# Performance work log

Measured on AMD Instinct MI355X. Metric: run time of the kernel, lower is better.

The kernel has to match this reference:

```python
import jax, jax.numpy as jnp
import numpy as np

B, S, D_MODEL, D_K, D_V, H = 4, 2048, 1024, 1024, 1024, 16


def setup_inputs() -> dict:
    key = jax.random.key(0)
    ks = jax.random.split(key, 8)
    std_qk = np.sqrt(2.0 / (D_MODEL + D_K)).astype(np.float32)
    std_v = np.sqrt(2.0 / (D_MODEL + D_V)).astype(np.float32)
    std_o = np.sqrt(2.0 / (D_V + D_MODEL)).astype(np.float32)  # xavier normal
    return {
        "Q": jax.random.normal(ks[0], (B, S, D_MODEL), jnp.float32),
        "K": jax.random.normal(ks[1], (B, S, D_MODEL), jnp.float32),
        "V": jax.random.normal(ks[2], (B, S, D_MODEL), jnp.float32),
        "Wq": jax.random.normal(ks[3], (D_MODEL, D_K), jnp.float32) * std_qk,
        "bq": jnp.zeros((D_K,), jnp.float32),
        "Wk": jax.random.normal(ks[4], (D_MODEL, D_K), jnp.float32) * std_qk,
        "bk": jnp.zeros((D_K,), jnp.float32),
        "Wv": jax.random.normal(ks[5], (D_MODEL, D_V), jnp.float32) * std_v,
        "bv": jnp.zeros((D_V,), jnp.float32),
        "Wo": jax.random.normal(ks[6], (D_V, D_MODEL), jnp.float32) * std_o,
        "bo": jnp.zeros((D_MODEL,), jnp.float32),
    }


def reference(Q, K, V, Wq, bq, Wk, bk, Wv, bv, Wo, bo):
    b, s, _ = Q.shape
    hd = D_K // H  # per-head dim
    # separate QKV projections
    q = (Q @ Wq + bq).reshape(b, s, H, hd)
    k = (K @ Wk + bk).reshape(b, s, H, hd)
    v = (V @ Wv + bv).reshape(b, s, H, D_V // H)
    # scaled dot-product attention per head
    scale = 1.0 / jnp.sqrt(jnp.asarray(hd, Q.dtype))
    scores = jnp.einsum("bqhd,bkhd->bhqk", q, k) * scale
    attn = jax.nn.softmax(scores, axis=-1)
    o = jnp.einsum("bhqk,bkhd->bqhd", attn, v).reshape(b, s, D_V)
    # output projection
    return o @ Wo + bo
```

## Files before the change

### kernel.cpp

```cpp
#include <hip/hip_runtime.h>
#include <hip/hip_bf16.h>
#include <stdint.h>


#define B_  4
#define S_  2048
#define DM  1024
#define H_  16
#define HD  64
#define BH  (B_ * H_)

typedef __attribute__((ext_vector_type(8))) short short8;
typedef __attribute__((ext_vector_type(4))) float f32x4;

union U8 { short8 v; ushort u[8]; };

__device__ __forceinline__ ushort f2bf(float f) {
  union { float f; uint32_t i; } x; x.f = f;
  uint32_t r = (x.i + 0x7FFFu + ((x.i >> 16) & 1u)) >> 16;
  return (ushort)r;
}

__device__ __forceinline__ uint32_t cvt_pk_bf16(float a, float b) {
  uint32_t r;
  asm("v_cvt_pk_bf16_f32 %0, %1, %2" : "=v"(r) : "v"(a), "v"(b));
  return r;
}

__device__ __forceinline__ float exp2f_fast(float x) {
  float r;
  asm("v_exp_f32 %0, %1" : "=v"(r) : "v"(x));
  return r;
}

__device__ __forceinline__ void glds16(const ushort* g, ushort* l) {
  __builtin_amdgcn_global_load_lds(
      (const __attribute__((address_space(1))) void*)g,
      (__attribute__((address_space(3))) void*)l, 16, 0, 0);
}

#define MAX3(a, b, c) fmaxf(fmaxf((a), (b)), (c))

__global__ __launch_bounds__(256) void transposeW4(
    const float* __restrict__ s0, const float* __restrict__ s1,
    const float* __restrict__ s2, const float* __restrict__ s3,
    ushort* __restrict__ dbase) {
  __shared__ __align__(16) ushort tile[64][72];
  const int t = threadIdx.x;
  const int bx = blockIdx.x & 15;
  const int by = blockIdx.x >> 4;
  const int wsel = blockIdx.y;
  const float* src = wsel == 0 ? s0 : (wsel == 1 ? s1 : (wsel == 2 ? s2 : s3));
  ushort* dst = dbase + (size_t)wsel * 1024 * 1024;
#pragma unroll
  for (int i = 0; i < 2; i++) {
    int e = (i * 256 + t) * 8;
    int r = e >> 6, c = e & 63;
    const float* sp = src + (size_t)(by * 64 + r) * 1024 + bx * 64 + c;
    float4 a = ((const float4*)sp)[0];
    float4 b = ((const float4*)sp)[1];
    tile[r][c + 0] = f2bf(a.x); tile[r][c + 1] = f2bf(a.y);
    tile[r][c + 2] = f2bf(a.z); tile[r][c + 3] = f2bf(a.w);
    tile[r][c + 4] = f2bf(b.x); tile[r][c + 5] = f2bf(b.y);
    tile[r][c + 6] = f2bf(b.z); tile[r][c + 7] = f2bf(b.w);
  }
  __syncthreads();
#pragma unroll
  for (int i = 0; i < 2; i++) {
    int e = (i * 256 + t) * 8;
    int r = e >> 6, c = e & 63;
    U8 st;
#pragma unroll
    for (int j = 0; j < 8; j++) st.u[j] = tile[c + j][r];
    *(short8*)(dst + (size_t)(bx * 64 + r) * 1024 + by * 64 + c) = st.v;
  }
}

__global__ __launch_bounds__(256, 2) void gemm_qkv(
    const float* __restrict__ Qa, const float* __restrict__ Ka, const float* __restrict__ Va,
    const ushort* __restrict__ WT,
    const float* __restrict__ bq, const float* __restrict__ bk, const float* __restrict__ bv,
    ushort* __restrict__ qws, ushort* __restrict__ kws, ushort* __restrict__ vt) {
  __shared__ __align__(16) ushort lA[128 * 32];
  __shared__ __align__(16) ushort lB[128 * 32];
  const int z = blockIdx.z;
  const float* Ap = z == 0 ? Qa : (z == 1 ? Ka : Va);
  const ushort* BT = WT + (size_t)z * 1024 * 1024;
  const float* bias = z == 0 ? bq : (z == 1 ? bk : bv);
  const float oscale = z == 0 ? 0.18033688f : 1.0f;
  const int t = threadIdx.x;
  const int lane = t & 63;
  const int w = t >> 6;
  const int wr = w >> 1, wc = w & 1;
  const int bm0 = blockIdx.x * 128;
  const int bn0 = blockIdx.y * 128;
  f32x4 acc[4][4] = {};

  const int arow = t >> 2;
  const int acol = (t & 3) * 8;
  const float* fA0 = Ap + (size_t)(bm0 + arow) * 1024 + acol;
  const float* fA1 = Ap + (size_t)(bm0 + 64 + arow) * 1024 + acol;
  const ushort* gB0 = BT + (size_t)(bn0 + arow) * 1024 + acol;
  const ushort* gB1 = BT + (size_t)(bn0 + 64 + arow) * 1024 + acol;

  for (int k0 = 0; k0 < 1024; k0 += 32) {
    if (k0) __syncthreads();
    float4 x0 = ((const float4*)(fA0 + k0))[0];
    float4 x1 = ((const float4*)(fA0 + k0))[1];
    float4 y0 = ((const float4*)(fA1 + k0))[0];
    float4 y1 = ((const float4*)(fA1 + k0))[1];
    union { short8 v; uint32_t u[4]; } s0, s1;
    s0.u[0] = cvt_pk_bf16(x0.x, x0.y); s0.u[1] = cvt_pk_bf16(x0.z, x0.w);
    s0.u[2] = cvt_pk_bf16(x1.x, x1.y); s0.u[3] = cvt_pk_bf16(x1.z, x1.w);
    s1.u[0] = cvt_pk_bf16(y0.x, y0.y); s1.u[1] = cvt_pk_bf16(y0.z, y0.w);
    s1.u[2] = cvt_pk_bf16(y1.x, y1.y); s1.u[3] = cvt_pk_bf16(y1.z, y1.w);
    *(short8*)&lA[t * 8] = s0.v;
    *(short8*)&lA[2048 + t * 8] = s1.v;
    glds16(gB0 + k0, &lB[t * 8]);
    glds16(gB1 + k0, &lB[2048 + t * 8]);
    __syncthreads();
    short8 af[4], bf[4];
#pragma unroll
    for (int i = 0; i < 4; i++)
      af[i] = *(const short8*)&lA[(wr * 64 + i * 16 + (lane & 15)) * 32 + (lane >> 4) * 8];
#pragma unroll
    for (int j = 0; j < 4; j++)
      bf[j] = *(const short8*)&lB[(wc * 64 + j * 16 + (lane & 15)) * 32 + (lane >> 4) * 8];
#pragma unroll
    for (int i = 0; i < 4; i++)
#pragma unroll
      for (int j = 0; j < 4; j++)
        acc[i][j] = __builtin_amdgcn_mfma_f32_16x16x32_bf16(af[i], bf[j], acc[i][j], 0, 0, 0);
  }

  const int r0 = (lane >> 4) * 4;
#pragma unroll
  for (int j = 0; j < 4; j++) {
    const int col = bn0 + wc * 64 + j * 16 + (lane & 15);
    const float bc = bias[col];
#pragma unroll
    for (int i = 0; i < 4; i++) {
      const int row = bm0 + wr * 64 + i * 16 + r0;
      const int bb = row >> 11, s = row & 2047;
      const int hh = col >> 6, d = col & 63;
      if (z == 2) {
        uint32_t p01 = cvt_pk_bf16(acc[i][j][0] + bc, acc[i][j][1] + bc);
        uint32_t p23 = cvt_pk_bf16(acc[i][j][2] + bc, acc[i][j][3] + bc);
        ushort* vtb = vt + (((size_t)bb * H_ + hh) * HD + d) * (size_t)S_;
        const int sc = (s & 63) >> 2;
        *(uint2*)(vtb + (s & ~63) + ((sc ^ (d & 15)) << 2)) = (uint2){p01, p23};
      } else {
        ushort* dst = z == 0 ? qws : kws;
#pragma unroll
        for (int r = 0; r < 4; r++) {
          float val = (acc[i][j][r] + bc) * oscale;
          dst[(((size_t)bb * H_ + hh) * S_ + (s + r)) * HD + d] = f2bf(val);
        }
      }
    }
  }
}

__global__ __launch_bounds__(256, 2) void gemm_out(
    const ushort* __restrict__ Ap, const ushort* __restrict__ BT,
    const float* __restrict__ bias, float* __restrict__ Cp) {
  __shared__ __align__(16) ushort lA[128 * 32];
  __shared__ __align__(16) ushort lB[128 * 32];
  const int t = threadIdx.x;
  const int lane = t & 63;
  const int w = t >> 6;
  const int wr = w >> 1, wc = w & 1;
  const int bm0 = blockIdx.x * 128;
  const int bn0 = blockIdx.y * 128;
  f32x4 acc[4][4] = {};

  const int arow = t >> 2;
  const int acol = (t & 3) * 8;
  const ushort* gA0 = Ap + (size_t)(bm0 + arow) * 1024 + acol;
  const ushort* gA1 = Ap + (size_t)(bm0 + 64 + arow) * 1024 + acol;
  const ushort* gB0 = BT + (size_t)(bn0 + arow) * 1024 + acol;
  const ushort* gB1 = BT + (size_t)(bn0 + 64 + arow) * 1024 + acol;

  for (int k0 = 0; k0 < 1024; k0 += 32) {
    if (k0) __syncthreads();
    glds16(gA0 + k0, &lA[t * 8]);
    glds16(gA1 + k0, &lA[2048 + t * 8]);
    glds16(gB0 + k0, &lB[t * 8]);
    glds16(gB1 + k0, &lB[2048 + t * 8]);
    __syncthreads();
    short8 af[4], bf[4];
#pragma unroll
    for (int i = 0; i < 4; i++)
      af[i] = *(const short8*)&lA[(wr * 64 + i * 16 + (lane & 15)) * 32 + (lane >> 4) * 8];
#pragma unroll
    for (int j = 0; j < 4; j++)
      bf[j] = *(const short8*)&lB[(wc * 64 + j * 16 + (lane & 15)) * 32 + (lane >> 4) * 8];
#pragma unroll
    for (int i = 0; i < 4; i++)
#pragma unroll
      for (int j = 0; j < 4; j++)
        acc[i][j] = __builtin_amdgcn_mfma_f32_16x16x32_bf16(af[i], bf[j], acc[i][j], 0, 0, 0);
  }

  const int r0 = (lane >> 4) * 4;
#pragma unroll
  for (int j = 0; j < 4; j++) {
    const int col = bn0 + wc * 64 + j * 16 + (lane & 15);
    const float bc = bias[col];
#pragma unroll
    for (int i = 0; i < 4; i++) {
      const int row = bm0 + wr * 64 + i * 16 + r0;
#pragma unroll
      for (int r = 0; r < 4; r++)
        Cp[(size_t)(row + r) * 1024 + col] = acc[i][j][r] + bc;
    }
  }
}

__global__ __launch_bounds__(256, 2) void attn(
    const ushort* __restrict__ q, const ushort* __restrict__ k,
    const ushort* __restrict__ vt, ushort* __restrict__ o) {
  __shared__ __align__(16) ushort kbuf[2][4096];
  __shared__ __align__(16) ushort vbuf[2][4096];
  const int t = threadIdx.x;
  const int lane = t & 63;
  const int w = t >> 6;
  const int L = ((blockIdx.x & 7) << 6) + (blockIdx.x >> 3);
  const int bh = L >> 3;
  const int q0 = (L & 7) * 256;
  const int b = bh >> 4, h = bh & 15;
  const int l15 = lane & 15;
  const int g = lane >> 4;

  const ushort* kbase  = k  + (size_t)bh * S_ * HD;
  const ushort* vtbase = vt + (size_t)bh * HD * S_;

  short8 qf[4][2];
#pragma unroll
  for (int qi = 0; qi < 4; qi++) {
    const ushort* qp = q + ((size_t)bh * S_ + q0 + w * 64 + qi * 16 + l15) * HD + g * 8;
    qf[qi][0] = *(const short8*)qp;
    qf[qi][1] = *(const short8*)(qp + 32);
  }

  short8 onesf;
#pragma unroll
  for (int j = 0; j < 8; j++) onesf[j] = (short)0x3F80;

  float m_r[4] = {-1e30f, -1e30f, -1e30f, -1e30f};
  f32x4 l_acc[4];
  f32x4 o_acc[4][4];
#pragma unroll
  for (int qi = 0; qi < 4; qi++) {
    l_acc[qi] = (f32x4){0.f, 0.f, 0.f, 0.f};
#pragma unroll
    for (int cb = 0; cb < 4; cb++) o_acc[qi][cb] = (f32x4){0.f, 0.f, 0.f, 0.f};
  }

  int vo[2][2];
#pragma unroll
  for (int ks = 0; ks < 2; ks++) {
    vo[ks][0] = ((8 * ks + g) ^ l15) << 2;
    vo[ks][1] = ((8 * ks + 4 + g) ^ l15) << 2;
  }

  auto STAGE = [&](int sel_, int kv0) {
#pragma unroll
    for (int i = 0; i < 2; i++) {
      int c = i * 256 + t;
      int row = c >> 3;
      int cc = (c & 7) ^ (row & 7);
      glds16(kbase + (size_t)(kv0 + row) * HD + cc * 8, &kbuf[sel_][c * 8]);
      glds16(vtbase + (size_t)row * S_ + kv0 + (c & 7) * 8, &vbuf[sel_][c * 8]);
    }
  };

  STAGE(0, 0);
  __syncthreads();

  int sel = 0;
  for (int kv0 = 0; kv0 < S_; kv0 += 64, sel ^= 1) {
    if (kv0 + 64 < S_) STAGE(sel ^ 1, kv0 + 64);

    f32x4 sc[4][4];
#pragma unroll
    for (int qi = 0; qi < 4; qi++)
#pragma unroll
      for (int cb = 0; cb < 4; cb++) sc[qi][cb] = (f32x4){0.f, 0.f, 0.f, 0.f};
    __builtin_amdgcn_s_setprio(1);
#pragma unroll
    for (int cb = 0; cb < 4; cb++) {
      const int row = cb * 16 + l15;
      const int r7 = row & 7;
      short8 kf0 = *(const short8*)&kbuf[sel][(row * 8 + (g ^ r7)) * 8];
      short8 kf1 = *(const short8*)&kbuf[sel][(row * 8 + ((4 + g) ^ r7)) * 8];
#pragma unroll
      for (int qi = 0; qi < 4; qi++) {
        sc[qi][cb] = __builtin_amdgcn_mfma_f32_16x16x32_bf16(kf0, qf[qi][0], sc[qi][cb], 0, 0, 0);
        sc[qi][cb] = __builtin_amdgcn_mfma_f32_16x16x32_bf16(kf1, qf[qi][1], sc[qi][cb], 0, 0, 0);
      }
    }
    __builtin_amdgcn_s_setprio(0);

    union PB { short8 v; uint32_t u[4]; } pbq[4][2];
#pragma unroll
    for (int qi = 0; qi < 4; qi++) {
      const float m = m_r[qi];
#pragma unroll
      for (int cb = 0; cb < 4; cb++) {
        float p0 = exp2f_fast(sc[qi][cb][0] - m);
        float p1 = exp2f_fast(sc[qi][cb][1] - m);
        float p2 = exp2f_fast(sc[qi][cb][2] - m);
        float p3 = exp2f_fast(sc[qi][cb][3] - m);
        pbq[qi][cb >> 1].u[(cb & 1) * 2 + 0] = cvt_pk_bf16(p0, p1);
        pbq[qi][cb >> 1].u[(cb & 1) * 2 + 1] = cvt_pk_bf16(p2, p3);
      }
      float z0 = MAX3(sc[qi][0][0], sc[qi][0][1], sc[qi][0][2]);
      float z1 = MAX3(sc[qi][0][3], sc[qi][1][0], sc[qi][1][1]);
      float z2 = MAX3(sc[qi][1][2], sc[qi][1][3], sc[qi][2][0]);
      float z3 = MAX3(sc[qi][2][1], sc[qi][2][2], sc[qi][2][3]);
      float z4 = MAX3(sc[qi][3][0], sc[qi][3][1], sc[qi][3][2]);
      float mx = MAX3(MAX3(z0, z1, z2), fmaxf(z3, z4), sc[qi][3][3]);
      mx = fmaxf(mx, __shfl_xor(mx, 16));
      mx = fmaxf(mx, __shfl_xor(mx, 32));

      const float THR = 11.5415603f;
      if (!__all(mx <= m + THR)) {
        float mn = fmaxf(m, mx);
        float fct = exp2f_fast(m - mn);
        m_r[qi] = mn;
        l_acc[qi] *= fct;
#pragma unroll
        for (int cb = 0; cb < 4; cb++)
#pragma unroll
          for (int r = 0; r < 4; r++) o_acc[qi][cb][r] *= fct;
#pragma unroll
        for (int cb = 0; cb < 4; cb++) {
          float p0 = exp2f_fast(sc[qi][cb][0] - mn);
          float p1 = exp2f_fast(sc[qi][cb][1] - mn);
          float p2 = exp2f_fast(sc[qi][cb][2] - mn);
          float p3 = exp2f_fast(sc[qi][cb][3] - mn);
          pbq[qi][cb >> 1].u[(cb & 1) * 2 + 0] = cvt_pk_bf16(p0, p1);
          pbq[qi][cb >> 1].u[(cb & 1) * 2 + 1] = cvt_pk_bf16(p2, p3);
        }
      }
    }

    __builtin_amdgcn_s_setprio(1);
#pragma unroll
    for (int ks = 0; ks < 2; ks++) {
#pragma unroll
      for (int qi = 0; qi < 4; qi++)
        l_acc[qi] = __builtin_amdgcn_mfma_f32_16x16x32_bf16(onesf, pbq[qi][ks].v, l_acc[qi], 0, 0, 0);
#pragma unroll
      for (int cb = 0; cb < 4; cb++) {
        const ushort* vb = &vbuf[sel][(cb * 16 + l15) * 64];
        union { short8 v; uint2 d2[2]; } vv;
        vv.d2[0] = *(const uint2*)(vb + vo[ks][0]);
        vv.d2[1] = *(const uint2*)(vb + vo[ks][1]);
#pragma unroll
        for (int qi = 0; qi < 4; qi++)
          o_acc[qi][cb] = __builtin_amdgcn_mfma_f32_16x16x32_bf16(vv.v, pbq[qi][ks].v, o_acc[qi][cb], 0, 0, 0);
      }
    }
    __builtin_amdgcn_s_setprio(0);
    __syncthreads();
  }

#pragma unroll
  for (int qi = 0; qi < 4; qi++) {
    const float inv = 1.f / l_acc[qi][0];
    ushort* ob = o + ((size_t)b * S_ + q0 + w * 64 + qi * 16 + l15) * DM + h * HD + 4 * g;
#pragma unroll
    for (int cb = 0; cb < 4; cb++) {
      uint2 st;
      st.x = cvt_pk_bf16(o_acc[qi][cb][0] * inv, o_acc[qi][cb][1] * inv);
      st.y = cvt_pk_bf16(o_acc[qi][cb][2] * inv, o_acc[qi][cb][3] * inv);
      *(uint2*)(ob + cb * 16) = st;
    }
  }
}

extern "C" void kernel_launch(void* const* d_in, const int* in_sizes, int n_in,
                              void* d_out, int out_size, void* d_ws, size_t ws_size,
                              hipStream_t stream) {
  const float* Q  = (const float*)d_in[0];
  const float* K  = (const float*)d_in[1];
  const float* V  = (const float*)d_in[2];
  const float* Wq = (const float*)d_in[3];
  const float* bq = (const float*)d_in[4];
  const float* Wk = (const float*)d_in[5];
  const float* bk = (const float*)d_in[6];
  const float* Wv = (const float*)d_in[7];
  const float* bv = (const float*)d_in[8];
  const float* Wo = (const float*)d_in[9];
  const float* bo = (const float*)d_in[10];
  float* out = (float*)d_out;
  ushort* ws = (ushort*)d_ws;

  const size_t WN = (size_t)1024 * 1024;
  const size_t PN = (size_t)B_ * S_ * DM;
  ushort* wT  = ws;
  ushort* woT = ws + 3 * WN;
  ushort* qws = ws + 4 * WN;
  ushort* kws = qws + PN;
  ushort* ows = kws + PN;
  ushort* vt  = (ushort*)d_out;

  transposeW4<<<dim3(256, 4), 256, 0, stream>>>(Wq, Wk, Wv, Wo, wT);

  gemm_qkv<<<dim3(64, 8, 3), 256, 0, stream>>>(Q, K, V, wT, bq, bk, bv, qws, kws, vt);

  attn<<<BH * 8, 256, 0, stream>>>(qws, kws, vt, ows);

  gemm_out<<<dim3(64, 8), 256, 0, stream>>>(ows, woT, bo, out);
}
```

Baseline: 196.4 us.

## Prefetch next A tile in projection GEMM and double KV tile size in attention

In the projection GEMM, the fp32 A-tile loads for the next k-step are issued into registers right after the barrier, so global latency overlaps the MFMA work. In attention, each staged K/V tile grows from 64 to 128 keys and is processed as two 64-key halves, halving the number of barriers and stage calls per sequence. This doubles the attention kernel's LDS footprint to 64KB per block, which may reduce occupancy, and the prefetch adds register pressure to the GEMM. The V tile layout changes to 128-wide rows, and the existing XOR read pattern is reused within each half.

Result: faster. 190.9 us (-2.8%).

```diff
diff --git a/kernel.cpp b/kernel.cpp
--- a/kernel.cpp
+++ b/kernel.cpp
@@ -103,22 +103,29 @@
   const ushort* gB0 = BT + (size_t)(bn0 + arow) * 1024 + acol;
   const ushort* gB1 = BT + (size_t)(bn0 + 64 + arow) * 1024 + acol;
 
+  float4 px0 = ((const float4*)fA0)[0];
+  float4 px1 = ((const float4*)fA0)[1];
+  float4 py0 = ((const float4*)fA1)[0];
+  float4 py1 = ((const float4*)fA1)[1];
+
   for (int k0 = 0; k0 < 1024; k0 += 32) {
     if (k0) __syncthreads();
-    float4 x0 = ((const float4*)(fA0 + k0))[0];
-    float4 x1 = ((const float4*)(fA0 + k0))[1];
-    float4 y0 = ((const float4*)(fA1 + k0))[0];
-    float4 y1 = ((const float4*)(fA1 + k0))[1];
     union { short8 v; uint32_t u[4]; } s0, s1;
-    s0.u[0] = cvt_pk_bf16(x0.x, x0.y); s0.u[1] = cvt_pk_bf16(x0.z, x0.w);
-    s0.u[2] = cvt_pk_bf16(x1.x, x1.y); s0.u[3] = cvt_pk_bf16(x1.z, x1.w);
-    s1.u[0] = cvt_pk_bf16(y0.x, y0.y); s1.u[1] = cvt_pk_bf16(y0.z, y0.w);
-    s1.u[2] = cvt_pk_bf16(y1.x, y1.y); s1.u[3] = cvt_pk_bf16(y1.z, y1.w);
+    s0.u[0] = cvt_pk_bf16(px0.x, px0.y); s0.u[1] = cvt_pk_bf16(px0.z, px0.w);
+    s0.u[2] = cvt_pk_bf16(px1.x, px1.y); s0.u[3] = cvt_pk_bf16(px1.z, px1.w);
+    s1.u[0] = cvt_pk_bf16(py0.x, py0.y); s1.u[1] = cvt_pk_bf16(py0.z, py0.w);
+    s1.u[2] = cvt_pk_bf16(py1.x, py1.y); s1.u[3] = cvt_pk_bf16(py1.z, py1.w);
     *(short8*)&lA[t * 8] = s0.v;
     *(short8*)&lA[2048 + t * 8] = s1.v;
     glds16(gB0 + k0, &lB[t * 8]);
     glds16(gB1 + k0, &lB[2048 + t * 8]);
     __syncthreads();
+    if (k0 + 32 < 1024) {
+      px0 = ((const float4*)(fA0 + k0 + 32))[0];
+      px1 = ((const float4*)(fA0 + k0 + 32))[1];
+      py0 = ((const float4*)(fA1 + k0 + 32))[0];
+      py1 = ((const float4*)(fA1 + k0 + 32))[1];
+    }
     short8 af[4], bf[4];
 #pragma unroll
     for (int i = 0; i < 4; i++)
@@ -220,8 +227,8 @@
 __global__ __launch_bounds__(256, 2) void attn(
     const ushort* __restrict__ q, const ushort* __restrict__ k,
     const ushort* __restrict__ vt, ushort* __restrict__ o) {
-  __shared__ __align__(16) ushort kbuf[2][4096];
-  __shared__ __align__(16) ushort vbuf[2][4096];
+  __shared__ __align__(16) ushort kbuf[2][8192];
+  __shared__ __align__(16) ushort vbuf[2][8192];
   const int t = threadIdx.x;
   const int lane = t & 63;
   const int w = t >> 6;
@@ -266,12 +273,14 @@
 
   auto STAGE = [&](int sel_, int kv0) {
 #pragma unroll
-    for (int i = 0; i < 2; i++) {
+    for (int i = 0; i < 4; i++) {
       int c = i * 256 + t;
-      int row = c >> 3;
-      int cc = (c & 7) ^ (row & 7);
-      glds16(kbase + (size_t)(kv0 + row) * HD + cc * 8, &kbuf[sel_][c * 8]);
-      glds16(vtbase + (size_t)row * S_ + kv0 + (c & 7) * 8, &vbuf[sel_][c * 8]);
+      int krow = c >> 3;
+      int kcc = (c & 7) ^ (krow & 7);
+      glds16(kbase + (size_t)(kv0 + krow) * HD + kcc * 8, &kbuf[sel_][c * 8]);
+      int d = c >> 4;
+      int voff = ((c >> 3) & 1) * 64 + (c & 7) * 8;
+      glds16(vtbase + (size_t)d * S_ + kv0 + voff, &vbuf[sel_][c * 8]);
     }
   };
 
@@ -279,91 +288,94 @@
   __syncthreads();
 
   int sel = 0;
-  for (int kv0 = 0; kv0 < S_; kv0 += 64, sel ^= 1) {
-    if (kv0 + 64 < S_) STAGE(sel ^ 1, kv0 + 64);
-
-    f32x4 sc[4][4];
-#pragma unroll
-    for (int qi = 0; qi < 4; qi++)
-#pragma unroll
-      for (int cb = 0; cb < 4; cb++) sc[qi][cb] = (f32x4){0.f, 0.f, 0.f, 0.f};
-    __builtin_amdgcn_s_setprio(1);
-#pragma unroll
-    for (int cb = 0; cb < 4; cb++) {
-      const int row = cb * 16 + l15;
-      const int r7 = row & 7;
-      short8 kf0 = *(const short8*)&kbuf[sel][(row * 8 + (g ^ r7)) * 8];
-      short8 kf1 = *(const short8*)&kbuf[sel][(row * 8 + ((4 + g) ^ r7)) * 8];
+  for (int kv0 = 0; kv0 < S_; kv0 += 128, sel ^= 1) {
+    if (kv0 + 128 < S_) STAGE(sel ^ 1, kv0 + 128);
+
+#pragma unroll
+    for (int hb = 0; hb < 2; hb++) {
+      f32x4 sc[4][4];
+#pragma unroll
+      for (int qi = 0; qi < 4; qi++)
+#pragma unroll
+        for (int cb = 0; cb < 4; cb++) sc[qi][cb] = (f32x4){0.f, 0.f, 0.f, 0.f};
+      __builtin_amdgcn_s_setprio(1);
+#pragma unroll
+      for (int cb = 0; cb < 4; cb++) {
+        const int row = hb * 64 + cb * 16 + l15;
+        const int r7 = row & 7;
+        short8 kf0 = *(const short8*)&kbuf[sel][(row * 8 + (g ^ r7)) * 8];
+        short8 kf1 = *(const short8*)&kbuf[sel][(row * 8 + ((4 + g) ^ r7)) * 8];
+#pragma unroll
+        for (int qi = 0; qi < 4; qi++) {
+          sc[qi][cb] = __builtin_amdgcn_mfma_f32_16x16x32_bf16(kf0, qf[qi][0], sc[qi][cb], 0, 0, 0);
+          sc[qi][cb] = __builtin_amdgcn_mfma_f32_16x16x32_bf16(kf1, qf[qi][1], sc[qi][cb], 0, 0, 0);
+        }
+      }
+      __builtin_amdgcn_s_setprio(0);
+
+      union PB { short8 v; uint32_t u[4]; } pbq[4][2];
 #pragma unroll
       for (int qi = 0; qi < 4; qi++) {
-        sc[qi][cb] = __builtin_amdgcn_mfma_f32_16x16x32_bf16(kf0, qf[qi][0], sc[qi][cb], 0, 0, 0);
-        sc[qi][cb] = __builtin_amdgcn_mfma_f32_16x16x32_bf16(kf1, qf[qi][1], sc[qi][cb], 0, 0, 0);
-      }
-    }
-    __builtin_amdgcn_s_setprio(0);
-
-    union PB { short8 v; uint32_t u[4]; } pbq[4][2];
-#pragma unroll
-    for (int qi = 0; qi < 4; qi++) {
-      const float m = m_r[qi];
-#pragma unroll
-      for (int cb = 0; cb < 4; cb++) {
-        float p0 = exp2f_fast(sc[qi][cb][0] - m);
-        float p1 = exp2f_fast(sc[qi][cb][1] - m);
-        float p2 = exp2f_fast(sc[qi][cb][2] - m);
-        float p3 = exp2f_fast(sc[qi][cb][3] - m);
-        pbq[qi][cb >> 1].u[(cb & 1) * 2 + 0] = cvt_pk_bf16(p0, p1);
-        pbq[qi][cb >> 1].u[(cb & 1) * 2 + 1] = cvt_pk_bf16(p2, p3);
-      }
-      float z0 = MAX3(sc[qi][0][0], sc[qi][0][1], sc[qi][0][2]);
-      float z1 = MAX3(sc[qi][0][3], sc[qi][1][0], sc[qi][1][1]);
-      float z2 = MAX3(sc[qi][1][2], sc[qi][1][3], sc[qi][2][0]);
-      float z3 = MAX3(sc[qi][2][1], sc[qi][2][2], sc[qi][2][3]);
-      float z4 = MAX3(sc[qi][3][0], sc[qi][3][1], sc[qi][3][2]);
-      float mx = MAX3(MAX3(z0, z1, z2), fmaxf(z3, z4), sc[qi][3][3]);
-      mx = fmaxf(mx, __shfl_xor(mx, 16));
-      mx = fmaxf(mx, __shfl_xor(mx, 32));
-
-      const float THR = 11.5415603f;
-      if (!__all(mx <= m + THR)) {
-        float mn = fmaxf(m, mx);
-        float fct = exp2f_fast(m - mn);
-        m_r[qi] = mn;
-        l_acc[qi] *= fct;
-#pragma unroll
-        for (int cb = 0; cb < 4; cb++)
-#pragma unroll
-          for (int r = 0; r < 4; r++) o_acc[qi][cb][r] *= fct;
+        const float m = m_r[qi];
 #pragma unroll
         for (int cb = 0; cb < 4; cb++) {
-          float p0 = exp2f_fast(sc[qi][cb][0] - mn);
-          float p1 = exp2f_fast(sc[qi][cb][1] - mn);
-          float p2 = exp2f_fast(sc[qi][cb][2] - mn);
-          float p3 = exp2f_fast(sc[qi][cb][3] - mn);
+          float p0 = exp2f_fast(sc[qi][cb][0] - m);
+          float p1 = exp2f_fast(sc[qi][cb][1] - m);
+          float p2 = exp2f_fast(sc[qi][cb][2] - m);
+          float p3 = exp2f_fast(sc[qi][cb][3] - m);
           pbq[qi][cb >> 1].u[(cb & 1) * 2 + 0] = cvt_pk_bf16(p0, p1);
           pbq[qi][cb >> 1].u[(cb & 1) * 2 + 1] = cvt_pk_bf16(p2, p3);
         }
+        float z0 = MAX3(sc[qi][0][0], sc[qi][0][1], sc[qi][0][2]);
+        float z1 = MAX3(sc[qi][0][3], sc[qi][1][0], sc[qi][1][1]);
+        float z2 = MAX3(sc[qi][1][2], sc[qi][1][3], sc[qi][2][0]);
+        float z3 = MAX3(sc[qi][2][1], sc[qi][2][2], sc[qi][2][3]);
+        float z4 = MAX3(sc[qi][3][0], sc[qi][3][1], sc[qi][3][2]);
+        float mx = MAX3(MAX3(z0, z1, z2), fmaxf(z3, z4), sc[qi][3][3]);
+        mx = fmaxf(mx, __shfl_xor(mx, 16));
+        mx = fmaxf(mx, __shfl_xor(mx, 32));
+
+        const float THR = 11.5415603f;
+        if (!__all(mx <= m + THR)) {
+          float mn = fmaxf(m, mx);
+          float fct = exp2f_fast(m - mn);
+          m_r[qi] = mn;
+          l_acc[qi] *= fct;
+#pragma unroll
+          for (int cb = 0; cb < 4; cb++)
+#pragma unroll
+            for (int r = 0; r < 4; r++) o_acc[qi][cb][r] *= fct;
+#pragma unroll
+          for (int cb = 0; cb < 4; cb++) {
+            float p0 = exp2f_fast(sc[qi][cb][0] - mn);
+            float p1 = exp2f_fast(sc[qi][cb][1] - mn);
+            float p2 = exp2f_fast(sc[qi][cb][2] - mn);
+            float p3 = exp2f_fast(sc[qi][cb][3] - mn);
+            pbq[qi][cb >> 1].u[(cb & 1) * 2 + 0] = cvt_pk_bf16(p0, p1);
+            pbq[qi][cb >> 1].u[(cb & 1) * 2 + 1] = cvt_pk_bf16(p2, p3);
+          }
+        }
       }
-    }
-
-    __builtin_amdgcn_s_setprio(1);
-#pragma unroll
-    for (int ks = 0; ks < 2; ks++) {
-#pragma unroll
-      for (int qi = 0; qi < 4; qi++)
-        l_acc[qi] = __builtin_amdgcn_mfma_f32_16x16x32_bf16(onesf, pbq[qi][ks].v, l_acc[qi], 0, 0, 0);
-#pragma unroll
-      for (int cb = 0; cb < 4; cb++) {
-        const ushort* vb = &vbuf[sel][(cb * 16 + l15) * 64];
-        union { short8 v; uint2 d2[2]; } vv;
-        vv.d2[0] = *(const uint2*)(vb + vo[ks][0]);
-        vv.d2[1] = *(const uint2*)(vb + vo[ks][1]);
+
+      __builtin_amdgcn_s_setprio(1);
+#pragma unroll
+      for (int ks = 0; ks < 2; ks++) {
 #pragma unroll
         for (int qi = 0; qi < 4; qi++)
-          o_acc[qi][cb] = __builtin_amdgcn_mfma_f32_16x16x32_bf16(vv.v, pbq[qi][ks].v, o_acc[qi][cb], 0, 0, 0);
+          l_acc[qi] = __builtin_amdgcn_mfma_f32_16x16x32_bf16(onesf, pbq[qi][ks].v, l_acc[qi], 0, 0, 0);
+#pragma unroll
+        for (int cb = 0; cb < 4; cb++) {
+          const ushort* vb = &vbuf[sel][(cb * 16 + l15) * 128 + hb * 64];
+          union { short8 v; uint2 d2[2]; } vv;
+          vv.d2[0] = *(const uint2*)(vb + vo[ks][0]);
+          vv.d2[1] = *(const uint2*)(vb + vo[ks][1]);
+#pragma unroll
+          for (int qi = 0; qi < 4; qi++)
+            o_acc[qi][cb] = __builtin_amdgcn_mfma_f32_16x16x32_bf16(vv.v, pbq[qi][ks].v, o_acc[qi][cb], 0, 0, 0);
+        }
       }
-    }
-    __builtin_amdgcn_s_setprio(0);
+      __builtin_amdgcn_s_setprio(0);
+    }
     __syncthreads();
   }
 
```
